# Performance work log

Measured on AMD Instinct MI355X. Metric: run time of the kernel, lower is better.

The kernel has to match this reference:

```python
import jax, jax.numpy as jnp
import numpy as np

Q, N, FDIM, HDIM = 4096, 1024, 64, 128


def setup_inputs() -> dict:
    key = jax.random.key(0)
    ks = jax.random.split(key, 7)
    s = 0.05
    return {
        "query_points": jax.random.normal(ks[0], (Q, 3), dtype=jnp.float32),
        "node_features": jax.random.normal(ks[1], (N, FDIM), dtype=jnp.float32),
        "node_positions": jax.random.normal(ks[2], (N, 3), dtype=jnp.float32),
        # attention MLP: Linear(F+3 -> H), ReLU, Linear(H -> 1)
        "aW1": jax.random.normal(ks[3], (FDIM + 3, HDIM), dtype=jnp.float32) * s,
        "ab1": jnp.zeros((HDIM,), dtype=jnp.float32),
        "aW2": jax.random.normal(ks[4], (HDIM, 1), dtype=jnp.float32) * s,
        "ab2": jnp.zeros((1,), dtype=jnp.float32),
        # decoder MLP: Linear(F -> H), ReLU, Linear(H -> 3)
        "dW1": jax.random.normal(ks[5], (FDIM, HDIM), dtype=jnp.float32) * s,
        "db1": jnp.zeros((HDIM,), dtype=jnp.float32),
        "dW2": jax.random.normal(ks[6], (HDIM, 3), dtype=jnp.float32) * s,
        "db2": jnp.zeros((3,), dtype=jnp.float32),
    }


def reference(query_points, node_features, node_positions,
              aW1, ab1, aW2, ab2, dW1, db1, dW2, db2):
    F = node_features.shape[1]
    # pairwise offsets: [Q, N, 3]
    diff = query_points[:, None, :] - node_positions[None, :, :]
    # xy-plane distance -> inverse-distance weights: [Q, N, 1]
    dist = jnp.linalg.norm(diff[..., :2], axis=-1, keepdims=True)
    w = 1.0 / (dist + 1e-6)
    # attn MLP on concat([node_features, diff]); split W1 so the feature
    # part ([N,F]@[F,H]) is computed once instead of per query pair.
    h = jax.nn.relu(node_features @ aW1[:F] + diff @ aW1[F:] + ab1)  # [Q, N, H]
    score = h @ aW2 + ab2                                            # [Q, N, 1]
    attn = jax.nn.softmax(score * w, axis=1)                         # [Q, N, 1]
    agg = jnp.einsum('qn,nf->qf', attn[..., 0], node_features)       # [Q, F]
    return jax.nn.relu(agg @ dW1 + db1) @ dW2 + db2                  # [Q, 3]
```

## Files before the change

### kernel.cpp

```cpp
#include <hip/hip_runtime.h>
#include <math.h>

#define QN 4096
#define NN 1024
#define FD 64
#define HD 128

typedef float v2f __attribute__((ext_vector_type(2)));
typedef float v4f __attribute__((ext_vector_type(4)));

#define OFF_UT4   0
#define OFF_B     524288
#define OFF_VU    655360
#define OFF_VB    659456
#define OFF_L     660480
#define OFF_PM    4854784
#define OFF_PART  5116928
#define OFF_SPART 7214080

__global__ __launch_bounds__(256) void k0_prep(
    const float* __restrict__ qp, const float* __restrict__ nf,
    const float* __restrict__ npos, const float* __restrict__ aW1,
    const float* __restrict__ ab1, const float* __restrict__ aW2,
    float* __restrict__ B, float* __restrict__ UT4,
    float* __restrict__ vu, float* __restrict__ vb) {
  int bid = blockIdx.x, t = threadIdx.x;
  if (bid < 2048) {
    int idx = bid * 256 + t;
    int j = idx & 3, q = (idx >> 2) & 4095, h4 = idx >> 14;
    int h = h4 * 4 + j;
    float u = qp[q*3+0] * aW1[(FD+0)*HD + h]
            + qp[q*3+1] * aW1[(FD+1)*HD + h]
            + qp[q*3+2] * aW1[(FD+2)*HD + h];
    UT4[idx] = u;
  } else if (bid < 2560) {
    int i2 = (bid - 2048) * 256 + t;
    int n = i2 >> 7, h = i2 & 127;
    float s = ab1[h];
    #pragma unroll
    for (int f = 0; f < FD; ++f) s = fmaf(nf[n*FD+f], aW1[f*HD+h], s);
    s -= npos[n*3+0] * aW1[(FD+0)*HD + h]
       + npos[n*3+1] * aW1[(FD+1)*HD + h]
       + npos[n*3+2] * aW1[(FD+2)*HD + h];
    B[i2] = s;
    float pv = s * aW2[h];
    #pragma unroll
    for (int m = 1; m < 64; m <<= 1) pv += __shfl_xor(pv, m, 64);
    __shared__ float ps[4];
    if ((t & 63) == 0) ps[t >> 6] = pv;
    __syncthreads();
    if (t == 0)   vb[n] = ps[0] + ps[1];
    if (t == 128) vb[n] = ps[2] + ps[3];
  } else {
    int q = (bid - 2560) * 256 + t;
    float q0 = qp[q*3+0], q1 = qp[q*3+1], q2 = qp[q*3+2];
    float acc = 0.f;
    #pragma unroll
    for (int h = 0; h < HD; ++h) {
      float u = q0 * aW1[(FD+0)*HD + h]
              + q1 * aW1[(FD+1)*HD + h]
              + q2 * aW1[(FD+2)*HD + h];
      acc = fmaf(aW2[h], u, acc);
    }
    vu[q] = acc;
  }
}

#define LOADU(dst) { \
  _Pragma("unroll") for (int qq = 0; qq < 4; ++qq) { \
    dst[qq][0] = p0[qq*64]; \
    dst[qq][1] = p1[qq*64]; } \
  p0 += 8192; p1 += 8192; }

#define COMPUTE(u) { \
  _Pragma("unroll") for (int nn = 0; nn < 4; ++nn) { \
    v4f b0 = bsb[(nb + nn)*32]; \
    v4f b1 = bsb[(nb + nn)*32 + 1]; \
    v2f b01 = __builtin_shufflevector(b0, b0, 0, 1); \
    v2f b23 = __builtin_shufflevector(b0, b0, 2, 3); \
    v2f b45 = __builtin_shufflevector(b1, b1, 0, 1); \
    v2f b67 = __builtin_shufflevector(b1, b1, 2, 3); \
    _Pragma("unroll") for (int qq = 0; qq < 4; ++qq) { \
      v2f u01 = __builtin_shufflevector(u[qq][0], u[qq][0], 0, 1); \
      v2f u23 = __builtin_shufflevector(u[qq][0], u[qq][0], 2, 3); \
      v2f u45 = __builtin_shufflevector(u[qq][1], u[qq][1], 0, 1); \
      v2f u67 = __builtin_shufflevector(u[qq][1], u[qq][1], 2, 3); \
      v2f t0, t1, t2, t3; \
      asm("v_pk_add_f32 %0, %1, %2" : "=v"(t0) : "v"(u01), "v"(b01)); \
      asm("v_pk_add_f32 %0, %1, %2" : "=v"(t1) : "v"(u23), "v"(b23)); \
      asm("v_pk_add_f32 %0, %1, %2" : "=v"(t2) : "v"(u45), "v"(b45)); \
      asm("v_pk_add_f32 %0, %1, %2" : "=v"(t3) : "v"(u67), "v"(b67)); \
      float a = acc[qq][nn]; \
      a = fmaf(aw[0], __builtin_fabsf(t0.x), a); \
      a = fmaf(aw[1], __builtin_fabsf(t0.y), a); \
      a = fmaf(aw[2], __builtin_fabsf(t1.x), a); \
      a = fmaf(aw[3], __builtin_fabsf(t1.y), a); \
      a = fmaf(aw[4], __builtin_fabsf(t2.x), a); \
      a = fmaf(aw[5], __builtin_fabsf(t2.y), a); \
      a = fmaf(aw[6], __builtin_fabsf(t3.x), a); \
      a = fmaf(aw[7], __builtin_fabsf(t3.y), a); \
      acc[qq][nn] = a; } } \
  bsb += 2; aw += 8; }

__global__ __launch_bounds__(256) void k2_logits(
    const float* __restrict__ Bg, const float* __restrict__ UT4,
    const float* __restrict__ aW2, const float* __restrict__ ab2,
    const float* __restrict__ qp, const float* __restrict__ npos,
    const float* __restrict__ vu, const float* __restrict__ vb,
    float* __restrict__ L, float* __restrict__ pm) {
  __shared__ float Bs[16 * HD];
  __shared__ float red[4][4][64];
  const int q0 = blockIdx.x * 256, n0 = blockIdx.y * 16;
  const int t = threadIdx.x;
  {
    const float4* src = (const float4*)(Bg + n0 * HD);
    float4* dst = (float4*)Bs;
    #pragma unroll
    for (int r = 0; r < 2; ++r) dst[r*256 + t] = src[r*256 + t];
  }
  __syncthreads();
  const int lane = t & 63, w = t >> 6;
  const int nb = w * 4;

  float acc[4][4];
  #pragma unroll
  for (int qq = 0; qq < 4; ++qq)
    #pragma unroll
    for (int nn = 0; nn < 4; ++nn) acc[qq][nn] = 0.f;

  const v4f* p0 = (const v4f*)UT4 + q0 + lane;
  const v4f* p1 = p0 + 4096;
  const v4f* bsb = (const v4f*)Bs;
  const float* aw = aW2;

  v4f uA[4][2], uB4[4][2];
  LOADU(uA);
  #pragma unroll 1
  for (int hc = 0; hc < 14; hc += 2) {
    LOADU(uB4);
    COMPUTE(uA);
    LOADU(uA);
    COMPUTE(uB4);
  }
  LOADU(uB4);
  COMPUTE(uA);
  COMPUTE(uB4);

  const float bias2 = ab2[0];
  float qx[4], qy[4], vuq[4], m4[4];
  #pragma unroll
  for (int qq = 0; qq < 4; ++qq) {
    int q = q0 + qq*64 + lane;
    qx[qq] = qp[q*3+0];
    qy[qq] = qp[q*3+1];
    vuq[qq] = vu[q];
    m4[qq] = -3.4e38f;
  }
  #pragma unroll
  for (int nn = 0; nn < 4; ++nn) {
    int n = n0 + nb + nn;
    float px = npos[n*3+0], py = npos[n*3+1];
    float vbn = vb[n];
    #pragma unroll
    for (int qq = 0; qq < 4; ++qq) {
      float dx = qx[qq] - px, dy = qy[qq] - py;
      float wgt = 1.f / (sqrtf(dx*dx + dy*dy) + 1e-6f);
      float score = fmaf(0.5f, vuq[qq] + vbn + acc[qq][nn], bias2);
      float lg = score * wgt;
      L[n * QN + q0 + qq*64 + lane] = lg;
      m4[qq] = fmaxf(m4[qq], lg);
    }
  }
  #pragma unroll
  for (int qq = 0; qq < 4; ++qq) red[w][qq][lane] = m4[qq];
  __syncthreads();
  {
    int qq = t >> 6, ll = t & 63;
    float mm = fmaxf(fmaxf(red[0][qq][ll], red[1][qq][ll]),
                     fmaxf(red[2][qq][ll], red[3][qq][ll]));
    pm[blockIdx.y * QN + q0 + qq*64 + ll] = mm;
  }
}

__global__ __launch_bounds__(256) void k4_agg(
    const float* __restrict__ L, const float* __restrict__ pm,
    const float* __restrict__ nf, float* __restrict__ part,
    float* __restrict__ spart) {
  __shared__ float red[4][2][32][33];
  __shared__ float sred[4][33];
  int b = blockIdx.x;
  int qt = b & 127, c = b >> 7;
  int t = threadIdx.x, lane = t & 63, w = t >> 6;
  int qi = lane & 31, fh = lane >> 5;
  int q = qt * 32 + qi;

  float m = -3.4e38f;
  #pragma unroll
  for (int k = 0; k < 64; ++k) m = fmaxf(m, pm[k * QN + q]);

  float acc[32];
  #pragma unroll
  for (int f = 0; f < 32; ++f) acc[f] = 0.f;
  float s = 0.f;

  int nbase = c * 128 + w * 32;
  const float* Lp = L + (size_t)nbase * QN + q;

  float pre[4];
  #pragma unroll
  for (int j = 0; j < 4; ++j) pre[j] = Lp[(size_t)j * QN];

  #pragma unroll 4
  for (int i = 0; i < 32; ++i) {
    float cur = pre[i & 3];
    if (i < 28) pre[i & 3] = Lp[(size_t)(i + 4) * QN];
    float p = exp2f((cur - m) * 1.44269504088896f);
    s += p;
    const float4* nfr = (const float4*)(nf + (nbase + i) * FD + fh * 32);
    #pragma unroll
    for (int g = 0; g < 8; ++g) {
      float4 a = nfr[g];
      acc[g*4+0] = fmaf(p, a.x, acc[g*4+0]);
      acc[g*4+1] = fmaf(p, a.y, acc[g*4+1]);
      acc[g*4+2] = fmaf(p, a.z, acc[g*4+2]);
      acc[g*4+3] = fmaf(p, a.w, acc[g*4+3]);
    }
  }

  #pragma unroll
  for (int fi = 0; fi < 32; ++fi) red[w][fh][fi][qi] = acc[fi];
  if (fh == 0) sred[w][qi] = s;
  __syncthreads();
  #pragma unroll
  for (int k = 0; k < 8; ++k) {
    int idx = k * 256 + t;
    int qq = idx >> 6, f = idx & 63;
    int f1 = f >> 5, f0 = f & 31;
    float sum = red[0][f1][f0][qq] + red[1][f1][f0][qq]
              + red[2][f1][f0][qq] + red[3][f1][f0][qq];
    part[((size_t)c * QN + qt*32 + qq) * 64 + f] = sum;
  }
  if (t < 32) {
    spart[c * QN + qt*32 + t] = sred[0][t] + sred[1][t] + sred[2][t] + sred[3][t];
  }
}

__global__ __launch_bounds__(256) void k5_dec(
    const float* __restrict__ part, const float* __restrict__ spart,
    const float* __restrict__ dW1, const float* __restrict__ db1,
    const float* __restrict__ dW2, const float* __restrict__ db2,
    float* __restrict__ out) {
  __shared__ float agg[16][64];
  __shared__ float inv[16];
  __shared__ float h1s[16][128];
  int t = threadIdx.x;
  int qb = blockIdx.x * 16;
  if (t < 16) {
    float s = 0.f;
    #pragma unroll
    for (int c = 0; c < 8; ++c) s += spart[c*QN + qb + t];
    inv[t] = 1.f / s;
  }
  {
    int f = t & 63, qh = t >> 6;
    #pragma unroll
    for (int pass = 0; pass < 4; ++pass) {
      int qs = pass*4 + qh;
      float v = 0.f;
      #pragma unroll
      for (int c = 0; c < 8; ++c) v += part[((size_t)c*QN + qb + qs)*64 + f];
      agg[qs][f] = v;
    }
  }
  __syncthreads();
  {
    int h = t & 127, qg = t >> 7;
    #pragma unroll
    for (int k = 0; k < 8; ++k) {
      int qs = qg*8 + k;
      float a = 0.f;
      #pragma unroll
      for (int f = 0; f < 64; ++f) a = fmaf(agg[qs][f], dW1[f*HD + h], a);
      h1s[qs][h] = fmaxf(a * inv[qs] + db1[h], 0.f);
    }
  }
  __syncthreads();
  if (t < 48) {
    int qs = t / 3, o = t % 3;
    float a = db2[o];
    #pragma unroll
    for (int h = 0; h < HD; ++h) a = fmaf(h1s[qs][h], dW2[h*3 + o], a);
    out[(qb + qs)*3 + o] = a;
  }
}

extern "C" void kernel_launch(void* const* d_in, const int* in_sizes, int n_in,
                              void* d_out, int out_size, void* d_ws, size_t ws_size,
                              hipStream_t stream) {
  const float* qp   = (const float*)d_in[0];
  const float* nf   = (const float*)d_in[1];
  const float* npos = (const float*)d_in[2];
  const float* aW1  = (const float*)d_in[3];
  const float* ab1  = (const float*)d_in[4];
  const float* aW2  = (const float*)d_in[5];
  const float* ab2  = (const float*)d_in[6];
  const float* dW1  = (const float*)d_in[7];
  const float* db1  = (const float*)d_in[8];
  const float* dW2  = (const float*)d_in[9];
  const float* db2  = (const float*)d_in[10];

  float* ws    = (float*)d_ws;
  float* UT4   = ws + OFF_UT4;
  float* B     = ws + OFF_B;
  float* vu    = ws + OFF_VU;
  float* vb    = ws + OFF_VB;
  float* L     = ws + OFF_L;
  float* pm    = ws + OFF_PM;
  float* part  = ws + OFF_PART;
  float* spart = ws + OFF_SPART;

  hipLaunchKernelGGL(k0_prep, dim3(2576), dim3(256), 0, stream,
                     qp, nf, npos, aW1, ab1, aW2, B, UT4, vu, vb);
  hipLaunchKernelGGL(k2_logits, dim3(16, 64), dim3(256), 0, stream,
                     B, UT4, aW2, ab2, qp, npos, vu, vb, L, pm);
  hipLaunchKernelGGL(k4_agg, dim3(1024), dim3(256), 0, stream, L, pm, nf, part, spart);
  hipLaunchKernelGGL(k5_dec, dim3(256), dim3(256), 0, stream,
                     part, spart, dW1, db1, dW2, db2, (float*)d_out);
}
```

Baseline: 105.0 us.

## Fuse softmax aggregation and decoder MLP into one kernel per 8-query block

Merges the aggregation kernel and the decoder kernel into a single kernel. Each block handles 8 queries over all 1024 nodes, with four waves each covering 256 nodes and reducing through shared memory, and then runs the decoder MLP in the same block. This removes one launch and the global round trip of the partial aggregation and sum buffers. The trade-off is fewer blocks (512 instead of 1024) and a serial 256-iteration loop per thread. L loads now come from only 8 consecutive queries per wavefront, so they are less coalesced, which could reduce memory efficiency.

```diff
diff --git a/kernel.cpp b/kernel.cpp
--- a/kernel.cpp
+++ b/kernel.cpp
@@ -15,8 +15,6 @@
 #define OFF_VB    659456
 #define OFF_L     660480
 #define OFF_PM    4854784
-#define OFF_PART  5116928
-#define OFF_SPART 7214080
 
 __global__ __launch_bounds__(256) void k0_prep(
     const float* __restrict__ qp, const float* __restrict__ nf,
@@ -182,102 +180,81 @@
   }
 }
 
-__global__ __launch_bounds__(256) void k4_agg(
+__global__ __launch_bounds__(256) void kB_aggdec(
     const float* __restrict__ L, const float* __restrict__ pm,
-    const float* __restrict__ nf, float* __restrict__ part,
-    float* __restrict__ spart) {
-  __shared__ float red[4][2][32][33];
-  __shared__ float sred[4][33];
-  int b = blockIdx.x;
-  int qt = b & 127, c = b >> 7;
-  int t = threadIdx.x, lane = t & 63, w = t >> 6;
-  int qi = lane & 31, fh = lane >> 5;
-  int q = qt * 32 + qi;
-
-  float m = -3.4e38f;
-  #pragma unroll
-  for (int k = 0; k < 64; ++k) m = fmaxf(m, pm[k * QN + q]);
-
-  float acc[32];
-  #pragma unroll
-  for (int f = 0; f < 32; ++f) acc[f] = 0.f;
-  float s = 0.f;
-
-  int nbase = c * 128 + w * 32;
-  const float* Lp = L + (size_t)nbase * QN + q;
-
-  float pre[4];
-  #pragma unroll
-  for (int j = 0; j < 4; ++j) pre[j] = Lp[(size_t)j * QN];
-
-  #pragma unroll 4
-  for (int i = 0; i < 32; ++i) {
-    float cur = pre[i & 3];
-    if (i < 28) pre[i & 3] = Lp[(size_t)(i + 4) * QN];
-    float p = exp2f((cur - m) * 1.44269504088896f);
-    s += p;
-    const float4* nfr = (const float4*)(nf + (nbase + i) * FD + fh * 32);
-    #pragma unroll
-    for (int g = 0; g < 8; ++g) {
-      float4 a = nfr[g];
-      acc[g*4+0] = fmaf(p, a.x, acc[g*4+0]);
-      acc[g*4+1] = fmaf(p, a.y, acc[g*4+1]);
-      acc[g*4+2] = fmaf(p, a.z, acc[g*4+2]);
-      acc[g*4+3] = fmaf(p, a.w, acc[g*4+3]);
-    }
-  }
-
-  #pragma unroll
-  for (int fi = 0; fi < 32; ++fi) red[w][fh][fi][qi] = acc[fi];
-  if (fh == 0) sred[w][qi] = s;
-  __syncthreads();
-  #pragma unroll
-  for (int k = 0; k < 8; ++k) {
-    int idx = k * 256 + t;
-    int qq = idx >> 6, f = idx & 63;
-    int f1 = f >> 5, f0 = f & 31;
-    float sum = red[0][f1][f0][qq] + red[1][f1][f0][qq]
-              + red[2][f1][f0][qq] + red[3][f1][f0][qq];
-    part[((size_t)c * QN + qt*32 + qq) * 64 + f] = sum;
-  }
-  if (t < 32) {
-    spart[c * QN + qt*32 + t] = sred[0][t] + sred[1][t] + sred[2][t] + sred[3][t];
-  }
-}
-
-__global__ __launch_bounds__(256) void k5_dec(
-    const float* __restrict__ part, const float* __restrict__ spart,
+    const float* __restrict__ nf,
     const float* __restrict__ dW1, const float* __restrict__ db1,
     const float* __restrict__ dW2, const float* __restrict__ db2,
     float* __restrict__ out) {
-  __shared__ float agg[16][64];
-  __shared__ float inv[16];
-  __shared__ float h1s[16][128];
-  int t = threadIdx.x;
-  int qb = blockIdx.x * 16;
-  if (t < 16) {
-    float s = 0.f;
-    #pragma unroll
-    for (int c = 0; c < 8; ++c) s += spart[c*QN + qb + t];
-    inv[t] = 1.f / s;
-  }
-  {
-    int f = t & 63, qh = t >> 6;
-    #pragma unroll
-    for (int pass = 0; pass < 4; ++pass) {
-      int qs = pass*4 + qh;
-      float v = 0.f;
-      #pragma unroll
-      for (int c = 0; c < 8; ++c) v += part[((size_t)c*QN + qb + qs)*64 + f];
-      agg[qs][f] = v;
+  __shared__ float red[4][64][9];
+  __shared__ float sred[4][64];
+  __shared__ float agg[8][65];
+  __shared__ float inv[8];
+  __shared__ float h1s[8][128];
+  const int t = threadIdx.x, lane = t & 63, w = t >> 6;
+  const int qi = lane & 7, fh = lane >> 3;
+  const int qb = blockIdx.x * 8;
+  const int q = qb + qi;
+
+  float m = -3.4e38f;
+  #pragma unroll
+  for (int k = 0; k < 64; ++k) m = fmaxf(m, pm[k * QN + q]);
+
+  float acc[8];
+  #pragma unroll
+  for (int j = 0; j < 8; ++j) acc[j] = 0.f;
+  float s = 0.f;
+
+  const int n0w = w * 256;
+  const float* Lp = L + (size_t)n0w * QN + q;
+  const float4* nfp = (const float4*)(nf + n0w * FD + fh * 8);
+
+  float pre[4];
+  #pragma unroll
+  for (int j = 0; j < 4; ++j) pre[j] = Lp[(size_t)j * QN];
+
+  #pragma unroll 4
+  for (int i = 0; i < 256; ++i) {
+    float cur = pre[i & 3];
+    if (i < 252) pre[i & 3] = Lp[(size_t)(i + 4) * QN];
+    float p = exp2f((cur - m) * 1.44269504088896f);
+    s += p;
+    float4 a0 = nfp[i * 16];
+    float4 a1 = nfp[i * 16 + 1];
+    acc[0] = fmaf(p, a0.x, acc[0]);
+    acc[1] = fmaf(p, a0.y, acc[1]);
+    acc[2] = fmaf(p, a0.z, acc[2]);
+    acc[3] = fmaf(p, a0.w, acc[3]);
+    acc[4] = fmaf(p, a1.x, acc[4]);
+    acc[5] = fmaf(p, a1.y, acc[5]);
+    acc[6] = fmaf(p, a1.z, acc[6]);
+    acc[7] = fmaf(p, a1.w, acc[7]);
+  }
+
+  #pragma unroll
+  for (int j = 0; j < 8; ++j) red[w][lane][j] = acc[j];
+  sred[w][lane] = s;
+  __syncthreads();
+
+  if (t < 64) {
+    int tqi = t & 7, tfh = t >> 3;
+    #pragma unroll
+    for (int j = 0; j < 8; ++j) {
+      float v = red[0][t][j] + red[1][t][j] + red[2][t][j] + red[3][t][j];
+      agg[tqi][tfh * 8 + j] = v;
     }
   }
-  __syncthreads();
+  if (t < 8) {
+    float ssum = sred[0][t] + sred[1][t] + sred[2][t] + sred[3][t];
+    inv[t] = 1.f / ssum;
+  }
+  __syncthreads();
+
   {
     int h = t & 127, qg = t >> 7;
     #pragma unroll
-    for (int k = 0; k < 8; ++k) {
-      int qs = qg*8 + k;
+    for (int k = 0; k < 4; ++k) {
+      int qs = qg * 4 + k;
       float a = 0.f;
       #pragma unroll
       for (int f = 0; f < 64; ++f) a = fmaf(agg[qs][f], dW1[f*HD + h], a);
@@ -285,7 +262,7 @@
     }
   }
   __syncthreads();
-  if (t < 48) {
+  if (t < 24) {
     int qs = t / 3, o = t % 3;
     float a = db2[o];
     #pragma unroll
@@ -316,14 +293,11 @@
   float* vb    = ws + OFF_VB;
   float* L     = ws + OFF_L;
   float* pm    = ws + OFF_PM;
-  float* part  = ws + OFF_PART;
-  float* spart = ws + OFF_SPART;
 
   hipLaunchKernelGGL(k0_prep, dim3(2576), dim3(256), 0, stream,
                      qp, nf, npos, aW1, ab1, aW2, B, UT4, vu, vb);
   hipLaunchKernelGGL(k2_logits, dim3(16, 64), dim3(256), 0, stream,
                      B, UT4, aW2, ab2, qp, npos, vu, vb, L, pm);
-  hipLaunchKernelGGL(k4_agg, dim3(1024), dim3(256), 0, stream, L, pm, nf, part, spart);
-  hipLaunchKernelGGL(k5_dec, dim3(256), dim3(256), 0, stream,
-                     part, spart, dW1, db1, dW2, db2, (float*)d_out);
+  hipLaunchKernelGGL(kB_aggdec, dim3(512), dim3(256), 0, stream,
+                     L, pm, nf, dW1, db1, dW2, db2, (float*)d_out);
 }
```

Result: slower. 173.5 us (+65.3%).
